# Kernel tuning notes

Hardware: AMD Instinct MI355X
Metric: run time of the kernel (lower is better)

The kernel has to match this reference:

```python
import jax, jax.numpy as jnp
import numpy as np

N_HEADS = 12
EPS = 1e-6
H_DIM = 768


def setup_inputs() -> dict:
    key = jax.random.key(0)
    ks = jax.random.split(key, 10)
    B, M, T, C = 2, 64, 512, H_DIM
    x = jax.random.normal(ks[0], (B, M, T, C), dtype=jnp.float32)
    mask = jnp.ones((B, M, T), dtype=jnp.float32)
    s = 1.0 / np.sqrt(C)
    Wq = jax.random.normal(ks[1], (C, C), dtype=jnp.float32) * s
    bq = jax.random.normal(ks[2], (C,), dtype=jnp.float32) * 0.01
    Wk = jax.random.normal(ks[3], (C, C), dtype=jnp.float32) * s
    bk = jax.random.normal(ks[4], (C,), dtype=jnp.float32) * 0.01
    Wv = jax.random.normal(ks[5], (C, C), dtype=jnp.float32) * s
    bv = jax.random.normal(ks[6], (C,), dtype=jnp.float32) * 0.01
    Wp = jax.random.normal(ks[7], (C, C), dtype=jnp.float32) * s
    bp = jax.random.normal(ks[8], (C,), dtype=jnp.float32) * 0.01
    return {"x": x, "mask": mask, "Wq": Wq, "bq": bq, "Wk": Wk, "bk": bk,
            "Wv": Wv, "bv": bv, "Wp": Wp, "bp": bp}


def reference(x, mask, Wq, bq, Wk, bk, Wv, bv, Wp, bp):
    B, M, T, C = x.shape
    N, D = N_HEADS, C // N_HEADS
    # projections: nn.Linear -> x @ W.T + b, then [B,M,T,N,D] -> [B,M,N,T,D]
    q = (x @ Wq.T + bq).reshape(B, M, T, N, D).transpose(0, 1, 3, 2, 4)
    k = (x @ Wk.T + bk).reshape(B, M, T, N, D).transpose(0, 1, 3, 2, 4)
    v = (x @ Wv.T + bv).reshape(B, M, T, N, D).transpose(0, 1, 3, 2, 4)
    q = jax.nn.elu(q) + 1.0
    k = jax.nn.elu(k) + 1.0
    k = k * mask[:, :, None, :, None]
    # KtV[b,m,n,d,e] = sum_t k[b,m,n,t,d] * v[b,m,n,t,e]   (small [D,D] per head)
    KtV = jnp.einsum('bmntd,bmnte->bmnde', k, v)
    # Z[b,m,n,t] = 1 / (q . sum_t' k + eps)
    Z = 1.0 / (jnp.einsum('bmntd,bmnd->bmnt', q, k.sum(axis=-2)) + EPS)
    # torch code does Z.expand(...,T,D) @ KtV, which equals Z * KtV.sum(over d)
    S = KtV.sum(axis=-2)                       # [B,M,N,E]
    V = Z[..., None] * S[:, :, :, None, :]     # [B,M,N,T,E]
    V = V.transpose(0, 1, 3, 2, 4).reshape(B, M, T, N * D)
    out = V @ Wp.T + bp
    return out
```

## Files before the change

kernel.cpp:

```cpp
#include <hip/hip_runtime.h>
#include <hip/hip_bf16.h>
#include <stdint.h>

typedef short short8 __attribute__((ext_vector_type(8)));
typedef float f32x4 __attribute__((ext_vector_type(4)));

#define EPS_Z 1e-6f

__device__ __forceinline__ unsigned short f2bf(float f) {
  uint32_t b = __float_as_uint(f);
  b += 0x7FFFu + ((b >> 16) & 1u);
  return (unsigned short)(b >> 16);
}
__device__ __forceinline__ float bf2f(unsigned short u) {
  return __uint_as_float(((uint32_t)u) << 16);
}

__device__ __forceinline__ void gl16(const unsigned short* g, unsigned short* l) {
  __builtin_amdgcn_global_load_lds(
      (const __attribute__((address_space(1))) unsigned int*)g,
      (__attribute__((address_space(3))) unsigned int*)l, 16, 0, 0);
}

__global__ __launch_bounds__(256) void k_cvt_all(
    const float* __restrict__ x, const float* __restrict__ Wk,
    const float* __restrict__ Wq, unsigned short* __restrict__ xbf,
    unsigned short* __restrict__ Wkbf, unsigned short* __restrict__ Wqbf) {
  const int bid = blockIdx.x;
  const float* in;
  unsigned short* out;
  int base;
  if (bid < 24576)      { in = x;  out = xbf;  base = bid; }
  else if (bid < 24864) { in = Wk; out = Wkbf; base = bid - 24576; }
  else                  { in = Wq; out = Wqbf; base = bid - 24864; }
  const int i = (base * 256 + threadIdx.x) * 8;
  float4 a = *(const float4*)(in + i);
  float4 b = *(const float4*)(in + i + 4);
  union { unsigned short u[8]; short8 v; } r;
  r.u[0] = f2bf(a.x); r.u[1] = f2bf(a.y); r.u[2] = f2bf(a.z); r.u[3] = f2bf(a.w);
  r.u[4] = f2bf(b.x); r.u[5] = f2bf(b.y); r.u[6] = f2bf(b.z); r.u[7] = f2bf(b.w);
  *(short8*)(out + i) = r.v;
}

__global__ __launch_bounds__(256, 2) void k_projqk(
    const unsigned short* __restrict__ xbf,
    const unsigned short* __restrict__ Wkbf,
    const unsigned short* __restrict__ Wqbf,
    const float* __restrict__ bk,
    const float* __restrict__ bq,
    const float* __restrict__ mask,
    float* __restrict__ kd,
    float* __restrict__ ksum_part,
    unsigned short* __restrict__ qbf)
{
  __shared__ unsigned short Ab[128][64];
  __shared__ unsigned short Bkb[128][64];
  __shared__ unsigned short Bqb[128][64];
  __shared__ float rowf[128];
  __shared__ float kcol[2][128];

  const int tid = threadIdx.x;
  const int lane = tid & 63;
  const int wid = tid >> 6;
  const int wr = wid >> 1, wc = wid & 1;
  const int flat = blockIdx.x;
  const int swz = (flat & 7) * 384 + (flat >> 3);
  const int colTile = swz % 6;
  const int rowTile = swz / 6;
  const int bm = rowTile >> 2;
  const int trow = rowTile & 3;
  const size_t rowBase = (size_t)rowTile * 128;
  const int colBase = colTile * 128;
  const int lrow = lane & 15;
  const int lgrp = lane >> 4;

  if (tid < 128) rowf[tid] = mask[bm * 512 + trow * 128 + tid];

  f32x4 ak[4][4] = {};
  f32x4 aq[4][4] = {};

  for (int kt = 0; kt < 12; ++kt) {
    const int k0 = kt * 64;
    __syncthreads();
#pragma unroll
    for (int c = 0; c < 4; ++c) {
      const int chunk = c * 256 + tid;
      const int r = chunk >> 3;
      const int cc = chunk & 7;
      const int scc = cc ^ (r & 7);
      const int ldst = c * 2048 + wid * 512;
      gl16(xbf + (rowBase + r) * 768 + k0 + scc * 8, &Ab[0][0] + ldst);
      gl16(Wkbf + (size_t)(colBase + r) * 768 + k0 + scc * 8, &Bkb[0][0] + ldst);
      gl16(Wqbf + (size_t)(colBase + r) * 768 + k0 + scc * 8, &Bqb[0][0] + ldst);
    }
    __syncthreads();
#pragma unroll
    for (int kk = 0; kk < 64; kk += 32) {
      short8 av[4], bvk[4], bvq[4];
#pragma unroll
      for (int rf = 0; rf < 4; ++rf) {
        const int row = wr * 64 + rf * 16 + lrow;
        const int cidx = ((kk >> 3) + lgrp) ^ (row & 7);
        av[rf] = *(const short8*)&Ab[row][cidx * 8];
      }
#pragma unroll
      for (int cf = 0; cf < 4; ++cf) {
        const int row = wc * 64 + cf * 16 + lrow;
        const int cidx = ((kk >> 3) + lgrp) ^ (row & 7);
        bvk[cf] = *(const short8*)&Bkb[row][cidx * 8];
        bvq[cf] = *(const short8*)&Bqb[row][cidx * 8];
      }
#pragma unroll
      for (int rf = 0; rf < 4; ++rf)
#pragma unroll
        for (int cf = 0; cf < 4; ++cf) {
          ak[rf][cf] = __builtin_amdgcn_mfma_f32_16x16x32_bf16(
              av[rf], bvk[cf], ak[rf][cf], 0, 0, 0);
          aq[rf][cf] = __builtin_amdgcn_mfma_f32_16x16x32_bf16(
              av[rf], bvq[cf], aq[rf][cf], 0, 0, 0);
        }
    }
  }

  float bkv[4], bqv[4];
#pragma unroll
  for (int cf = 0; cf < 4; ++cf) {
    bkv[cf] = bk[colBase + wc * 64 + cf * 16 + lrow];
    bqv[cf] = bq[colBase + wc * 64 + cf * 16 + lrow];
  }
#pragma unroll
  for (int rf = 0; rf < 4; ++rf)
#pragma unroll
    for (int cf = 0; cf < 4; ++cf)
#pragma unroll
      for (int j = 0; j < 4; ++j) {
        float v = ak[rf][cf][j] + bkv[cf];
        v = (v > 0.0f) ? (v + 1.0f) : __expf(v);
        ak[rf][cf][j] = v * rowf[wr * 64 + rf * 16 + lgrp * 4 + j];
        float u = aq[rf][cf][j] + bqv[cf];
        aq[rf][cf][j] = (u > 0.0f) ? (u + 1.0f) : __expf(u);
      }

  const int head = colTile * 2 + wc;

#pragma unroll
  for (int rf = 0; rf < 4; ++rf)
#pragma unroll
    for (int j = 0; j < 4; ++j) {
      float s = ak[rf][0][j] + ak[rf][1][j] + ak[rf][2][j] + ak[rf][3][j];
      s += __shfl_xor(s, 1, 64);
      s += __shfl_xor(s, 2, 64);
      s += __shfl_xor(s, 4, 64);
      s += __shfl_xor(s, 8, 64);
      if ((lane & 15) == 0) {
        const int t = trow * 128 + wr * 64 + rf * 16 + lgrp * 4 + j;
        kd[((size_t)bm * 512 + t) * 12 + head] = s;
      }
    }

#pragma unroll
  for (int cf = 0; cf < 4; ++cf) {
    float s = 0.f;
#pragma unroll
    for (int rf = 0; rf < 4; ++rf)
#pragma unroll
      for (int j = 0; j < 4; ++j) s += ak[rf][cf][j];
    s += __shfl_xor(s, 16, 64);
    s += __shfl_xor(s, 32, 64);
    if (lane < 16) kcol[wr][wc * 64 + cf * 16 + lane] = s;
  }

#pragma unroll
  for (int rf = 0; rf < 4; ++rf)
#pragma unroll
    for (int j = 0; j < 4; ++j) {
      const int t = trow * 128 + wr * 64 + rf * 16 + lgrp * 4 + j;
      unsigned short* qp = qbf + (((size_t)bm * 12 + head) * 512 + t) * 64 + lrow;
#pragma unroll
      for (int cf = 0; cf < 4; ++cf)
        qp[cf * 16] = f2bf(aq[rf][cf][j]);
    }

  __syncthreads();
  if (tid < 128)
    ksum_part[((size_t)bm * 4 + trow) * 768 + colBase + tid] =
        kcol[0][tid] + kcol[1][tid];
}

__global__ __launch_bounds__(256) void k_xkz(const unsigned short* __restrict__ xbf,
                                             const float* __restrict__ kd,
                                             float* __restrict__ xk_part,
                                             const unsigned short* __restrict__ qbf,
                                             const float* __restrict__ ksum_part,
                                             float* __restrict__ Z) {
  const int bid = blockIdx.x, tid = threadIdx.x;
  if (bid < 512) {
    __shared__ float kdl[128][12];
    const int bm = bid >> 2, ts = bid & 3;
    for (int i = tid; i < 128 * 12; i += 256)
      kdl[i / 12][i % 12] = kd[((size_t)bm * 512 + ts * 128 + i / 12) * 12 + (i % 12)];
    __syncthreads();
    if (tid < 192) {
      float a[12][4];
#pragma unroll
      for (int n = 0; n < 12; ++n)
#pragma unroll
        for (int j = 0; j < 4; ++j) a[n][j] = 0.f;
      const int c = tid * 4;
      const unsigned short* xp = xbf + ((size_t)bm * 512 + ts * 128) * 768 + c;
      for (int t = 0; t < 128; ++t) {
        ushort4 xv = *(const ushort4*)(xp + (size_t)t * 768);
        const float x0 = bf2f(xv.x), x1 = bf2f(xv.y), x2 = bf2f(xv.z), x3 = bf2f(xv.w);
#pragma unroll
        for (int n = 0; n < 12; ++n) {
          const float kv = kdl[t][n];
          a[n][0] += kv * x0; a[n][1] += kv * x1; a[n][2] += kv * x2; a[n][3] += kv * x3;
        }
      }
      float* op = xk_part + ((size_t)bm * 4 + ts) * 12 * 768 + c;
#pragma unroll
      for (int n = 0; n < 12; ++n)
        *(float4*)(op + (size_t)n * 768) = make_float4(a[n][0], a[n][1], a[n][2], a[n][3]);
    }
  } else {
    __shared__ float ksum_l[768];
    const int b2 = bid - 512;
    const int bm = b2 >> 2, ts = b2 & 3;
    for (int i = tid; i < 768; i += 256) {
      const float* kp = ksum_part + (size_t)bm * 3072 + i;
      ksum_l[i] = kp[0] + kp[768] + kp[1536] + kp[2304];
    }
    __syncthreads();
#pragma unroll
    for (int i = 0; i < 6; ++i) {
      const int task = i * 256 + tid;
      const int n = task >> 7;
      const int t = ts * 128 + (task & 127);
      const unsigned short* qp = qbf + (((size_t)bm * 12 + n) * 512 + t) * 64;
      const float* kp = &ksum_l[n * 64];
      float s = 0.f;
#pragma unroll
      for (int c = 0; c < 8; ++c) {
        short8 qv = *(const short8*)(qp + c * 8);
        s += bf2f((unsigned short)qv[0]) * kp[c * 8 + 0]
           + bf2f((unsigned short)qv[1]) * kp[c * 8 + 1]
           + bf2f((unsigned short)qv[2]) * kp[c * 8 + 2]
           + bf2f((unsigned short)qv[3]) * kp[c * 8 + 3]
           + bf2f((unsigned short)qv[4]) * kp[c * 8 + 4]
           + bf2f((unsigned short)qv[5]) * kp[c * 8 + 5]
           + bf2f((unsigned short)qv[6]) * kp[c * 8 + 6]
           + bf2f((unsigned short)qv[7]) * kp[c * 8 + 7];
      }
      Z[((size_t)bm * 12 + n) * 512 + t] = 1.0f / (s + EPS_Z);
    }
  }
}

__global__ __launch_bounds__(256) void k_sg(const float* __restrict__ ksum_part,
                                            const float* __restrict__ xk_part,
                                            const float* __restrict__ Wv,
                                            const float* __restrict__ bv,
                                            const float* __restrict__ Wp,
                                            float* __restrict__ G) {
  __shared__ __align__(16) float xk_l[768];
  __shared__ __align__(16) float S_l[64];
  __shared__ float kdsum_s;
  const int bm = blockIdx.x, n = blockIdx.y, tid = threadIdx.x;

  if (tid < 192) {
    const float* xp = xk_part + (size_t)bm * 4 * 9216 + n * 768 + tid * 4;
    float4 a = *(const float4*)(xp);
    float4 b = *(const float4*)(xp + 9216);
    float4 c = *(const float4*)(xp + 18432);
    float4 d = *(const float4*)(xp + 27648);
    *(float4*)&xk_l[tid * 4] = make_float4(a.x + b.x + c.x + d.x,
                                           a.y + b.y + c.y + d.y,
                                           a.z + b.z + c.z + d.z,
                                           a.w + b.w + c.w + d.w);
  } else {
    const int d = tid - 192;
    const float* kp = ksum_part + (size_t)bm * 4 * 768 + n * 64 + d;
    float s = kp[0] + kp[768] + kp[1536] + kp[2304];
    s += __shfl_xor(s, 1, 64);
    s += __shfl_xor(s, 2, 64);
    s += __shfl_xor(s, 4, 64);
    s += __shfl_xor(s, 8, 64);
    s += __shfl_xor(s, 16, 64);
    s += __shfl_xor(s, 32, 64);
    if (d == 0) kdsum_s = s;
  }
  __syncthreads();

  {
    const int e = tid >> 2, q = tid & 3;
    const float4* wv = (const float4*)(Wv + (size_t)(n * 64 + e) * 768 + q * 192);
    const float4* xp4 = (const float4*)(xk_l + q * 192);
    float s = 0.f;
#pragma unroll
    for (int i = 0; i < 48; ++i) {
      float4 w = wv[i], xx = xp4[i];
      s += w.x * xx.x + w.y * xx.y + w.z * xx.z + w.w * xx.w;
    }
    s += __shfl_xor(s, 1, 64);
    s += __shfl_xor(s, 2, 64);
    if (q == 0) S_l[e] = s + bv[n * 64 + e] * kdsum_s;
  }
  __syncthreads();

#pragma unroll
  for (int r = 0; r < 3; ++r) {
    const int p = r * 256 + tid;
    const float4* wp = (const float4*)(Wp + (size_t)p * 768 + n * 64);
    const float4* sp = (const float4*)S_l;
    float g = 0.f;
#pragma unroll
    for (int i = 0; i < 16; ++i) {
      float4 w = wp[i], s = sp[i];
      g += w.x * s.x + w.y * s.y + w.z * s.z + w.w * s.w;
    }
    G[((size_t)bm * 12 + n) * 768 + p] = g;
  }
}

__global__ __launch_bounds__(256) void k_out(const float* __restrict__ Z,
                                             const float* __restrict__ G,
                                             const float* __restrict__ bp,
                                             float* __restrict__ outp) {
  __shared__ __align__(16) float G_l[9216];
  __shared__ float Z_l[768];
  __shared__ __align__(16) float bp_l[768];
  const int bm = blockIdx.x;
  const int tbase = blockIdx.y * 64;
  const int tid = threadIdx.x;
  for (int i = tid; i < 9216; i += 256) G_l[i] = G[(size_t)bm * 9216 + i];
  for (int i = tid; i < 768; i += 256) {
    bp_l[i] = bp[i];
    Z_l[i] = Z[((size_t)bm * 12 + (i >> 6)) * 512 + tbase + (i & 63)];
  }
  __syncthreads();
  for (int it = 0; it < 48; ++it) {
    const int idx = it * 1024 + tid * 4;
    const int t = idx / 768;
    const int p = idx - t * 768;
    float4 o = *(const float4*)&bp_l[p];
#pragma unroll
    for (int n = 0; n < 12; ++n) {
      const float z = Z_l[n * 64 + t];
      const float4 g = *(const float4*)&G_l[n * 768 + p];
      o.x += z * g.x; o.y += z * g.y; o.z += z * g.z; o.w += z * g.w;
    }
    *(float4*)&outp[((size_t)bm * 512 + tbase + t) * 768 + p] = o;
  }
}

extern "C" void kernel_launch(void* const* d_in, const int* in_sizes, int n_in,
                              void* d_out, int out_size, void* d_ws, size_t ws_size,
                              hipStream_t stream) {
  const float* x    = (const float*)d_in[0];
  const float* mask = (const float*)d_in[1];
  const float* Wq   = (const float*)d_in[2];
  const float* bq   = (const float*)d_in[3];
  const float* Wk   = (const float*)d_in[4];
  const float* bk   = (const float*)d_in[5];
  const float* Wv   = (const float*)d_in[6];
  const float* bv   = (const float*)d_in[7];
  const float* Wp   = (const float*)d_in[8];
  const float* bp   = (const float*)d_in[9];
  float* outp = (float*)d_out;

  char* ws = (char*)d_ws;
  unsigned short* xbf  = (unsigned short*)(ws);
  unsigned short* Wkbf = (unsigned short*)(ws + 100663296);
  unsigned short* Wqbf = (unsigned short*)(ws + 101842944);
  float* kd        = (float*)(ws + 103022592);
  float* ksum_part = (float*)(ws + 106168320);
  float* xk_part   = (float*)(ws + 107741184);
  float* Zb        = (float*)(ws + 126615552);
  float* G         = (float*)(ws + 129761280);
  unsigned short* qbf = (unsigned short*)d_out;

  hipLaunchKernelGGL(k_cvt_all, dim3(25152), dim3(256), 0, stream,
                     x, Wk, Wq, xbf, Wkbf, Wqbf);
  hipLaunchKernelGGL(k_projqk, dim3(3072), dim3(256), 0, stream,
                     xbf, Wkbf, Wqbf, bk, bq, mask, kd, ksum_part, qbf);
  hipLaunchKernelGGL(k_xkz, dim3(1024), dim3(256), 0, stream,
                     xbf, kd, xk_part, qbf, ksum_part, Zb);
  hipLaunchKernelGGL(k_sg, dim3(128, 12), dim3(256), 0, stream,
                     ksum_part, xk_part, Wv, bv, Wp, G);
  hipLaunchKernelGGL(k_out, dim3(128, 8), dim3(256), 0, stream, Zb, G, bp, outp);
}
```

Baseline: 482.1 us.

## Double-buffer projqk LDS tiles and enlarge row tile to 256 with 512 threads

The Q/K projection GEMM kernel now stages the next K-slice into a second LDS buffer while MFMAs run on the current one, removing one barrier per iteration. The block tile grows from 128 to 256 rows with 8 waves, so each weight tile is reused across twice as many rows and the grid halves. ksum partials drop from 4 to 2 per batch-row, and downstream consumers are updated to match. LDS use roughly quadruples (about 130KB), which may cut occupancy well below the requested 2 blocks per CU.

```diff
diff --git a/kernel.cpp b/kernel.cpp
--- a/kernel.cpp
+++ b/kernel.cpp
@@ -42,7 +42,63 @@
   *(short8*)(out + i) = r.v;
 }
 
-__global__ __launch_bounds__(256, 2) void k_projqk(
+
+__device__ __forceinline__ void stage_tile(
+    const unsigned short* __restrict__ xbf,
+    const unsigned short* __restrict__ Wkbf,
+    const unsigned short* __restrict__ Wqbf,
+    size_t rowBase, int colBase, int k0, int tid,
+    unsigned short* Abuf, unsigned short* Kbuf, unsigned short* Qbuf) {
+#pragma unroll
+  for (int c = 0; c < 4; ++c) {
+    const int chunk = c * 512 + tid;
+    const int r = chunk >> 3;
+    const int scc = (chunk & 7) ^ (r & 7);
+    gl16(xbf + (rowBase + r) * 768 + k0 + scc * 8, Abuf + chunk * 8);
+  }
+#pragma unroll
+  for (int c = 0; c < 2; ++c) {
+    const int chunk = c * 512 + tid;
+    const int r = chunk >> 3;
+    const int scc = (chunk & 7) ^ (r & 7);
+    gl16(Wkbf + (size_t)(colBase + r) * 768 + k0 + scc * 8, Kbuf + chunk * 8);
+    gl16(Wqbf + (size_t)(colBase + r) * 768 + k0 + scc * 8, Qbuf + chunk * 8);
+  }
+}
+
+__device__ __forceinline__ void compute_tile(
+    const unsigned short* Abuf, const unsigned short* Kbuf,
+    const unsigned short* Qbuf, int wr, int wc, int lrow, int lgrp,
+    f32x4 (&ak)[4][4], f32x4 (&aq)[4][4]) {
+#pragma unroll
+  for (int kk = 0; kk < 64; kk += 32) {
+    short8 av[4], bvk[4], bvq[4];
+#pragma unroll
+    for (int rf = 0; rf < 4; ++rf) {
+      const int row = wr * 64 + rf * 16 + lrow;
+      const int cidx = ((kk >> 3) + lgrp) ^ (row & 7);
+      av[rf] = *(const short8*)(Abuf + row * 64 + cidx * 8);
+    }
+#pragma unroll
+    for (int cf = 0; cf < 4; ++cf) {
+      const int row = wc * 64 + cf * 16 + lrow;
+      const int cidx = ((kk >> 3) + lgrp) ^ (row & 7);
+      bvk[cf] = *(const short8*)(Kbuf + row * 64 + cidx * 8);
+      bvq[cf] = *(const short8*)(Qbuf + row * 64 + cidx * 8);
+    }
+#pragma unroll
+    for (int rf = 0; rf < 4; ++rf)
+#pragma unroll
+      for (int cf = 0; cf < 4; ++cf) {
+        ak[rf][cf] = __builtin_amdgcn_mfma_f32_16x16x32_bf16(
+            av[rf], bvk[cf], ak[rf][cf], 0, 0, 0);
+        aq[rf][cf] = __builtin_amdgcn_mfma_f32_16x16x32_bf16(
+            av[rf], bvq[cf], aq[rf][cf], 0, 0, 0);
+      }
+  }
+}
+
+__global__ __launch_bounds__(512, 2) void k_projqk(
     const unsigned short* __restrict__ xbf,
     const unsigned short* __restrict__ Wkbf,
     const unsigned short* __restrict__ Wqbf,
@@ -53,73 +109,48 @@
     float* __restrict__ ksum_part,
     unsigned short* __restrict__ qbf)
 {
-  __shared__ unsigned short Ab[128][64];
-  __shared__ unsigned short Bkb[128][64];
-  __shared__ unsigned short Bqb[128][64];
-  __shared__ float rowf[128];
-  __shared__ float kcol[2][128];
+  __shared__ unsigned short Ab[2][256][64];
+  __shared__ unsigned short Bkb[2][128][64];
+  __shared__ unsigned short Bqb[2][128][64];
+  __shared__ float rowf[256];
+  __shared__ float kcol[4][128];
 
   const int tid = threadIdx.x;
   const int lane = tid & 63;
   const int wid = tid >> 6;
-  const int wr = wid >> 1, wc = wid & 1;
+  const int wr = wid >> 1;
+  const int wc = wid & 1;
   const int flat = blockIdx.x;
-  const int swz = (flat & 7) * 384 + (flat >> 3);
+  const int swz = (flat & 7) * 192 + (flat >> 3);
   const int colTile = swz % 6;
   const int rowTile = swz / 6;
-  const int bm = rowTile >> 2;
-  const int trow = rowTile & 3;
-  const size_t rowBase = (size_t)rowTile * 128;
+  const int bm = rowTile >> 1;
+  const int half = rowTile & 1;
+  const size_t rowBase = (size_t)rowTile * 256;
   const int colBase = colTile * 128;
   const int lrow = lane & 15;
   const int lgrp = lane >> 4;
 
-  if (tid < 128) rowf[tid] = mask[bm * 512 + trow * 128 + tid];
+  if (tid < 256) rowf[tid] = mask[bm * 512 + half * 256 + tid];
 
   f32x4 ak[4][4] = {};
   f32x4 aq[4][4] = {};
 
-  for (int kt = 0; kt < 12; ++kt) {
-    const int k0 = kt * 64;
+  unsigned short* A0 = &Ab[0][0][0]; unsigned short* A1 = &Ab[1][0][0];
+  unsigned short* K0 = &Bkb[0][0][0]; unsigned short* K1 = &Bkb[1][0][0];
+  unsigned short* Q0 = &Bqb[0][0][0]; unsigned short* Q1 = &Bqb[1][0][0];
+
+  stage_tile(xbf, Wkbf, Wqbf, rowBase, colBase, 0, tid, A0, K0, Q0);
+  __syncthreads();
+#pragma unroll 1
+  for (int kt = 0; kt < 12; kt += 2) {
+    stage_tile(xbf, Wkbf, Wqbf, rowBase, colBase, (kt + 1) * 64, tid, A1, K1, Q1);
+    compute_tile(A0, K0, Q0, wr, wc, lrow, lgrp, ak, aq);
     __syncthreads();
-#pragma unroll
-    for (int c = 0; c < 4; ++c) {
-      const int chunk = c * 256 + tid;
-      const int r = chunk >> 3;
-      const int cc = chunk & 7;
-      const int scc = cc ^ (r & 7);
-      const int ldst = c * 2048 + wid * 512;
-      gl16(xbf + (rowBase + r) * 768 + k0 + scc * 8, &Ab[0][0] + ldst);
-      gl16(Wkbf + (size_t)(colBase + r) * 768 + k0 + scc * 8, &Bkb[0][0] + ldst);
-      gl16(Wqbf + (size_t)(colBase + r) * 768 + k0 + scc * 8, &Bqb[0][0] + ldst);
-    }
+    if (kt + 2 < 12)
+      stage_tile(xbf, Wkbf, Wqbf, rowBase, colBase, (kt + 2) * 64, tid, A0, K0, Q0);
+    compute_tile(A1, K1, Q1, wr, wc, lrow, lgrp, ak, aq);
     __syncthreads();
-#pragma unroll
-    for (int kk = 0; kk < 64; kk += 32) {
-      short8 av[4], bvk[4], bvq[4];
-#pragma unroll
-      for (int rf = 0; rf < 4; ++rf) {
-        const int row = wr * 64 + rf * 16 + lrow;
-        const int cidx = ((kk >> 3) + lgrp) ^ (row & 7);
-        av[rf] = *(const short8*)&Ab[row][cidx * 8];
-      }
-#pragma unroll
-      for (int cf = 0; cf < 4; ++cf) {
-        const int row = wc * 64 + cf * 16 + lrow;
-        const int cidx = ((kk >> 3) + lgrp) ^ (row & 7);
-        bvk[cf] = *(const short8*)&Bkb[row][cidx * 8];
-        bvq[cf] = *(const short8*)&Bqb[row][cidx * 8];
-      }
-#pragma unroll
-      for (int rf = 0; rf < 4; ++rf)
-#pragma unroll
-        for (int cf = 0; cf < 4; ++cf) {
-          ak[rf][cf] = __builtin_amdgcn_mfma_f32_16x16x32_bf16(
-              av[rf], bvk[cf], ak[rf][cf], 0, 0, 0);
-          aq[rf][cf] = __builtin_amdgcn_mfma_f32_16x16x32_bf16(
-              av[rf], bvq[cf], aq[rf][cf], 0, 0, 0);
-        }
-    }
   }
 
   float bkv[4], bqv[4];
@@ -153,7 +184,7 @@
       s += __shfl_xor(s, 4, 64);
       s += __shfl_xor(s, 8, 64);
       if ((lane & 15) == 0) {
-        const int t = trow * 128 + wr * 64 + rf * 16 + lgrp * 4 + j;
+        const int t = half * 256 + wr * 64 + rf * 16 + lgrp * 4 + j;
         kd[((size_t)bm * 512 + t) * 12 + head] = s;
       }
     }
@@ -174,7 +205,7 @@
   for (int rf = 0; rf < 4; ++rf)
 #pragma unroll
     for (int j = 0; j < 4; ++j) {
-      const int t = trow * 128 + wr * 64 + rf * 16 + lgrp * 4 + j;
+      const int t = half * 256 + wr * 64 + rf * 16 + lgrp * 4 + j;
       unsigned short* qp = qbf + (((size_t)bm * 12 + head) * 512 + t) * 64 + lrow;
 #pragma unroll
       for (int cf = 0; cf < 4; ++cf)
@@ -183,8 +214,8 @@
 
   __syncthreads();
   if (tid < 128)
-    ksum_part[((size_t)bm * 4 + trow) * 768 + colBase + tid] =
-        kcol[0][tid] + kcol[1][tid];
+    ksum_part[((size_t)bm * 2 + half) * 768 + colBase + tid] =
+        kcol[0][tid] + kcol[1][tid] + kcol[2][tid] + kcol[3][tid];
 }
 
 __global__ __launch_bounds__(256) void k_xkz(const unsigned short* __restrict__ xbf,
@@ -227,8 +258,8 @@
     const int b2 = bid - 512;
     const int bm = b2 >> 2, ts = b2 & 3;
     for (int i = tid; i < 768; i += 256) {
-      const float* kp = ksum_part + (size_t)bm * 3072 + i;
-      ksum_l[i] = kp[0] + kp[768] + kp[1536] + kp[2304];
+      const float* kp = ksum_part + (size_t)bm * 1536 + i;
+      ksum_l[i] = kp[0] + kp[768];
     }
     __syncthreads();
 #pragma unroll
@@ -279,8 +310,8 @@
                                            a.w + b.w + c.w + d.w);
   } else {
     const int d = tid - 192;
-    const float* kp = ksum_part + (size_t)bm * 4 * 768 + n * 64 + d;
-    float s = kp[0] + kp[768] + kp[1536] + kp[2304];
+    const float* kp = ksum_part + (size_t)bm * 1536 + n * 64 + d;
+    float s = kp[0] + kp[768];
     s += __shfl_xor(s, 1, 64);
     s += __shfl_xor(s, 2, 64);
     s += __shfl_xor(s, 4, 64);
@@ -381,7 +412,7 @@
 
   hipLaunchKernelGGL(k_cvt_all, dim3(25152), dim3(256), 0, stream,
                      x, Wk, Wq, xbf, Wkbf, Wqbf);
-  hipLaunchKernelGGL(k_projqk, dim3(3072), dim3(256), 0, stream,
+  hipLaunchKernelGGL(k_projqk, dim3(1536), dim3(512), 0, stream,
                      xbf, Wkbf, Wqbf, bk, bq, mask, kd, ksum_part, qbf);
   hipLaunchKernelGGL(k_xkz, dim3(1024), dim3(256), 0, stream,
                      xbf, kd, xk_part, qbf, ksum_part, Zb);
```

Result: no change. 481.3 us (-0.2%).

## Double-buffer QK projection tiles and split K/Q GEMMs across separate waves

Applied to the files above, without the earlier changes.

The fused Q/K projection kernel now double-buffers its LDS tiles: it prefetches the next k-slice with global_load_lds while the current one is multiplied, and uses explicit vmcnt waits plus barriers. Blocks grow to 512 threads, with four waves computing the K projection and four computing the Q projection, so each wave holds one accumulator set instead of two. The aim is to hide global-load latency and cut per-wave register pressure. In exchange, LDS use doubles to about 96KB per block and occupancy drops to one block per CU.

```diff
diff --git a/kernel.cpp b/kernel.cpp
--- a/kernel.cpp
+++ b/kernel.cpp
@@ -42,7 +42,52 @@
   *(short8*)(out + i) = r.v;
 }
 
-__global__ __launch_bounds__(256, 2) void k_projqk(
+
+__device__ __forceinline__ void stage_tile(
+    const unsigned short* __restrict__ xbf,
+    const unsigned short* __restrict__ Wkbf,
+    const unsigned short* __restrict__ Wqbf,
+    size_t rowBase, int colBase, int k0, int tid,
+    unsigned short* Abuf, unsigned short* Kbuf, unsigned short* Qbuf) {
+#pragma unroll
+  for (int c = 0; c < 2; ++c) {
+    const int chunk = c * 512 + tid;
+    const int r = chunk >> 3;
+    const int scc = (chunk & 7) ^ (r & 7);
+    gl16(xbf + (rowBase + r) * 768 + k0 + scc * 8, Abuf + chunk * 8);
+    gl16(Wkbf + (size_t)(colBase + r) * 768 + k0 + scc * 8, Kbuf + chunk * 8);
+    gl16(Wqbf + (size_t)(colBase + r) * 768 + k0 + scc * 8, Qbuf + chunk * 8);
+  }
+}
+
+__device__ __forceinline__ void compute_tile(
+    const unsigned short* Abuf, const unsigned short* Bbuf,
+    int wr, int wc, int lrow, int lgrp, f32x4 (&acc)[4][4]) {
+#pragma unroll
+  for (int kk = 0; kk < 64; kk += 32) {
+    short8 av[4], bv4[4];
+#pragma unroll
+    for (int rf = 0; rf < 4; ++rf) {
+      const int row = wr * 64 + rf * 16 + lrow;
+      const int cidx = ((kk >> 3) + lgrp) ^ (row & 7);
+      av[rf] = *(const short8*)(Abuf + row * 64 + cidx * 8);
+    }
+#pragma unroll
+    for (int cf = 0; cf < 4; ++cf) {
+      const int row = wc * 64 + cf * 16 + lrow;
+      const int cidx = ((kk >> 3) + lgrp) ^ (row & 7);
+      bv4[cf] = *(const short8*)(Bbuf + row * 64 + cidx * 8);
+    }
+#pragma unroll
+    for (int rf = 0; rf < 4; ++rf)
+#pragma unroll
+      for (int cf = 0; cf < 4; ++cf)
+        acc[rf][cf] = __builtin_amdgcn_mfma_f32_16x16x32_bf16(
+            av[rf], bv4[cf], acc[rf][cf], 0, 0, 0);
+  }
+}
+
+__global__ __launch_bounds__(512, 1) void k_projqk(
     const unsigned short* __restrict__ xbf,
     const unsigned short* __restrict__ Wkbf,
     const unsigned short* __restrict__ Wqbf,
@@ -53,16 +98,18 @@
     float* __restrict__ ksum_part,
     unsigned short* __restrict__ qbf)
 {
-  __shared__ unsigned short Ab[128][64];
-  __shared__ unsigned short Bkb[128][64];
-  __shared__ unsigned short Bqb[128][64];
+  __shared__ unsigned short Ab[2][128][64];
+  __shared__ unsigned short Bkb[2][128][64];
+  __shared__ unsigned short Bqb[2][128][64];
   __shared__ float rowf[128];
   __shared__ float kcol[2][128];
 
   const int tid = threadIdx.x;
   const int lane = tid & 63;
   const int wid = tid >> 6;
-  const int wr = wid >> 1, wc = wid & 1;
+  const int isQ = wid >> 2;
+  const int w2 = wid & 3;
+  const int wr = w2 >> 1, wc = w2 & 1;
   const int flat = blockIdx.x;
   const int swz = (flat & 7) * 384 + (flat >> 3);
   const int colTile = swz % 6;
@@ -76,110 +123,90 @@
 
   if (tid < 128) rowf[tid] = mask[bm * 512 + trow * 128 + tid];
 
-  f32x4 ak[4][4] = {};
-  f32x4 aq[4][4] = {};
-
+  f32x4 acc[4][4] = {};
+
+  unsigned short* Ac = &Ab[0][0][0];  unsigned short* An = &Ab[1][0][0];
+  unsigned short* Kc = &Bkb[0][0][0]; unsigned short* Kn = &Bkb[1][0][0];
+  unsigned short* Qc = &Bqb[0][0][0]; unsigned short* Qn = &Bqb[1][0][0];
+
+  stage_tile(xbf, Wkbf, Wqbf, rowBase, colBase, 0, tid, Ac, Kc, Qc);
+
+#pragma unroll 1
   for (int kt = 0; kt < 12; ++kt) {
-    const int k0 = kt * 64;
-    __syncthreads();
-#pragma unroll
-    for (int c = 0; c < 4; ++c) {
-      const int chunk = c * 256 + tid;
-      const int r = chunk >> 3;
-      const int cc = chunk & 7;
-      const int scc = cc ^ (r & 7);
-      const int ldst = c * 2048 + wid * 512;
-      gl16(xbf + (rowBase + r) * 768 + k0 + scc * 8, &Ab[0][0] + ldst);
-      gl16(Wkbf + (size_t)(colBase + r) * 768 + k0 + scc * 8, &Bkb[0][0] + ldst);
-      gl16(Wqbf + (size_t)(colBase + r) * 768 + k0 + scc * 8, &Bqb[0][0] + ldst);
-    }
-    __syncthreads();
-#pragma unroll
-    for (int kk = 0; kk < 64; kk += 32) {
-      short8 av[4], bvk[4], bvq[4];
-#pragma unroll
-      for (int rf = 0; rf < 4; ++rf) {
-        const int row = wr * 64 + rf * 16 + lrow;
-        const int cidx = ((kk >> 3) + lgrp) ^ (row & 7);
-        av[rf] = *(const short8*)&Ab[row][cidx * 8];
+    if (kt < 11) {
+      stage_tile(xbf, Wkbf, Wqbf, rowBase, colBase, (kt + 1) * 64, tid, An, Kn, Qn);
+      asm volatile("s_waitcnt vmcnt(6)" ::: "memory");
+    } else {
+      asm volatile("s_waitcnt vmcnt(0)" ::: "memory");
+    }
+    __builtin_amdgcn_s_barrier();
+    asm volatile("" ::: "memory");
+    compute_tile(Ac, isQ ? Qc : Kc, wr, wc, lrow, lgrp, acc);
+    asm volatile("" ::: "memory");
+    __builtin_amdgcn_s_barrier();
+    unsigned short* t;
+    t = Ac; Ac = An; An = t;
+    t = Kc; Kc = Kn; Kn = t;
+    t = Qc; Qc = Qn; Qn = t;
+  }
+
+  const float* bias = isQ ? bq : bk;
+  float bvv[4];
+#pragma unroll
+  for (int cf = 0; cf < 4; ++cf)
+    bvv[cf] = bias[colBase + wc * 64 + cf * 16 + lrow];
+#pragma unroll
+  for (int rf = 0; rf < 4; ++rf)
+#pragma unroll
+    for (int cf = 0; cf < 4; ++cf)
+#pragma unroll
+      for (int j = 0; j < 4; ++j) {
+        float v = acc[rf][cf][j] + bvv[cf];
+        v = (v > 0.0f) ? (v + 1.0f) : __expf(v);
+        if (!isQ) v *= rowf[wr * 64 + rf * 16 + lgrp * 4 + j];
+        acc[rf][cf][j] = v;
       }
-#pragma unroll
-      for (int cf = 0; cf < 4; ++cf) {
-        const int row = wc * 64 + cf * 16 + lrow;
-        const int cidx = ((kk >> 3) + lgrp) ^ (row & 7);
-        bvk[cf] = *(const short8*)&Bkb[row][cidx * 8];
-        bvq[cf] = *(const short8*)&Bqb[row][cidx * 8];
+
+  const int head = colTile * 2 + wc;
+
+  if (!isQ) {
+#pragma unroll
+    for (int rf = 0; rf < 4; ++rf)
+#pragma unroll
+      for (int j = 0; j < 4; ++j) {
+        float s = acc[rf][0][j] + acc[rf][1][j] + acc[rf][2][j] + acc[rf][3][j];
+        s += __shfl_xor(s, 1, 64);
+        s += __shfl_xor(s, 2, 64);
+        s += __shfl_xor(s, 4, 64);
+        s += __shfl_xor(s, 8, 64);
+        if ((lane & 15) == 0) {
+          const int t = trow * 128 + wr * 64 + rf * 16 + lgrp * 4 + j;
+          kd[((size_t)bm * 512 + t) * 12 + head] = s;
+        }
       }
 #pragma unroll
+    for (int cf = 0; cf < 4; ++cf) {
+      float s = 0.f;
+#pragma unroll
       for (int rf = 0; rf < 4; ++rf)
 #pragma unroll
-        for (int cf = 0; cf < 4; ++cf) {
-          ak[rf][cf] = __builtin_amdgcn_mfma_f32_16x16x32_bf16(
-              av[rf], bvk[cf], ak[rf][cf], 0, 0, 0);
-          aq[rf][cf] = __builtin_amdgcn_mfma_f32_16x16x32_bf16(
-              av[rf], bvq[cf], aq[rf][cf], 0, 0, 0);
-        }
-    }
-  }
-
-  float bkv[4], bqv[4];
-#pragma unroll
-  for (int cf = 0; cf < 4; ++cf) {
-    bkv[cf] = bk[colBase + wc * 64 + cf * 16 + lrow];
-    bqv[cf] = bq[colBase + wc * 64 + cf * 16 + lrow];
-  }
-#pragma unroll
-  for (int rf = 0; rf < 4; ++rf)
-#pragma unroll
-    for (int cf = 0; cf < 4; ++cf)
+        for (int j = 0; j < 4; ++j) s += acc[rf][cf][j];
+      s += __shfl_xor(s, 16, 64);
+      s += __shfl_xor(s, 32, 64);
+      if (lane < 16) kcol[wr][wc * 64 + cf * 16 + lane] = s;
+    }
+  } else {
+#pragma unroll
+    for (int rf = 0; rf < 4; ++rf)
 #pragma unroll
       for (int j = 0; j < 4; ++j) {
-        float v = ak[rf][cf][j] + bkv[cf];
-        v = (v > 0.0f) ? (v + 1.0f) : __expf(v);
-        ak[rf][cf][j] = v * rowf[wr * 64 + rf * 16 + lgrp * 4 + j];
-        float u = aq[rf][cf][j] + bqv[cf];
-        aq[rf][cf][j] = (u > 0.0f) ? (u + 1.0f) : __expf(u);
+        const int t = trow * 128 + wr * 64 + rf * 16 + lgrp * 4 + j;
+        unsigned short* qp = qbf + (((size_t)bm * 12 + head) * 512 + t) * 64 + lrow;
+#pragma unroll
+        for (int cf = 0; cf < 4; ++cf)
+          qp[cf * 16] = f2bf(acc[rf][cf][j]);
       }
-
-  const int head = colTile * 2 + wc;
-
-#pragma unroll
-  for (int rf = 0; rf < 4; ++rf)
-#pragma unroll
-    for (int j = 0; j < 4; ++j) {
-      float s = ak[rf][0][j] + ak[rf][1][j] + ak[rf][2][j] + ak[rf][3][j];
-      s += __shfl_xor(s, 1, 64);
-      s += __shfl_xor(s, 2, 64);
-      s += __shfl_xor(s, 4, 64);
-      s += __shfl_xor(s, 8, 64);
-      if ((lane & 15) == 0) {
-        const int t = trow * 128 + wr * 64 + rf * 16 + lgrp * 4 + j;
-        kd[((size_t)bm * 512 + t) * 12 + head] = s;
-      }
-    }
-
-#pragma unroll
-  for (int cf = 0; cf < 4; ++cf) {
-    float s = 0.f;
-#pragma unroll
-    for (int rf = 0; rf < 4; ++rf)
-#pragma unroll
-      for (int j = 0; j < 4; ++j) s += ak[rf][cf][j];
-    s += __shfl_xor(s, 16, 64);
-    s += __shfl_xor(s, 32, 64);
-    if (lane < 16) kcol[wr][wc * 64 + cf * 16 + lane] = s;
-  }
-
-#pragma unroll
-  for (int rf = 0; rf < 4; ++rf)
-#pragma unroll
-    for (int j = 0; j < 4; ++j) {
-      const int t = trow * 128 + wr * 64 + rf * 16 + lgrp * 4 + j;
-      unsigned short* qp = qbf + (((size_t)bm * 12 + head) * 512 + t) * 64 + lrow;
-#pragma unroll
-      for (int cf = 0; cf < 4; ++cf)
-        qp[cf * 16] = f2bf(aq[rf][cf][j]);
-    }
+  }
 
   __syncthreads();
   if (tid < 128)
@@ -381,7 +408,7 @@
 
   hipLaunchKernelGGL(k_cvt_all, dim3(25152), dim3(256), 0, stream,
                      x, Wk, Wq, xbf, Wkbf, Wqbf);
-  hipLaunchKernelGGL(k_projqk, dim3(3072), dim3(256), 0, stream,
+  hipLaunchKernelGGL(k_projqk, dim3(3072), dim3(512), 0, stream,
                      xbf, Wkbf, Wqbf, bk, bq, mask, kd, ksum_part, qbf);
   hipLaunchKernelGGL(k_xkz, dim3(1024), dim3(256), 0, stream,
                      xbf, kd, xk_part, qbf, ksum_part, Zb);
```

Result: slower. 569.7 us (+18.2%).
